# Kernel optimization log

Measured on AMD Instinct MI355X. Metric: run time of the kernel, lower is better.

The kernel has to match this reference:

```python
import jax, jax.numpy as jnp
import numpy as np

NUM_HEADS = 64
HEAD_DIM = 10  # forced by nn.Linear(10, 1)


def setup_inputs() -> dict:
    key = jax.random.key(0)
    kq, kk, kv, kw = jax.random.split(key, 4)
    B, T, M = 16, 4096, NUM_HEADS * HEAD_DIM
    return {
        "query": jax.random.normal(kq, (B, T, M), dtype=jnp.float32),
        "key": jax.random.normal(kk, (B, T, M), dtype=jnp.float32),
        "value": jax.random.normal(kv, (B, T, M), dtype=jnp.float32),
        "W": jax.random.normal(kw, (1, HEAD_DIM), dtype=jnp.float32) * 0.3,
        "b": jnp.zeros((1,), dtype=jnp.float32),
    }


def _to_heads(x):
    # torch: stack(split(x, head_dim, dim=2), dim=0) -> [H, B, T, D]
    B, T, M = x.shape
    return x.reshape(B, T, NUM_HEADS, HEAD_DIM).transpose(2, 0, 1, 3)


def reference(query, key, value, W, b):
    D = HEAD_DIM
    q = _to_heads(query)   # [H,B,T,D]
    k = _to_heads(key)     # [H,B,T,D]
    v = _to_heads(value)   # [H,B,T,D]
    # key.transpose(-1,-2).sum(3).unsqueeze(2): sum over T -> [H,B,1,D]
    k_sum = k.sum(axis=2, keepdims=True)
    attn = jax.nn.softmax(jnp.tanh(q * k_sum / np.float32(np.sqrt(D))), axis=-1)
    t = attn * v                          # [H,B,T,D]
    v_q = t.sum(axis=2)                   # [H,B,D]
    v_v = t.sum(axis=3).transpose(1, 0, 2)  # [B,H,T]
    # input_proj: Linear(10,1) on v_q*v_q (v_query == v_key == t summed over T)
    s = jnp.tanh((v_q * v_q) @ W.T + b)   # [H,B,1]
    s = jax.nn.softmax(s, axis=-1)        # softmax over size-1 dim (== ones)
    s = s.transpose(1, 0, 2)              # [B,H,1]
    return v_v * s                        # [B,H,T]
```

## Files before the change

### kernel.cpp

```cpp
#include <hip/hip_runtime.h>
#include <stdint.h>

#define BB 16
#define TT 4096
#define HH 64
#define MM 640

#define PADF4 41
#define ROWSF (PADF4 * 4)

__global__ void __launch_bounds__(256)
ksum_kernel(const float* __restrict__ key, float* __restrict__ ksum) {
    int g = blockIdx.x * blockDim.x + threadIdx.x;
    int b = g / 160;
    int c = g % 160;
    int t0 = blockIdx.y * 32;

    const float4* p = reinterpret_cast<const float4*>(key)
                    + (size_t)b * TT * 160 + (size_t)t0 * 160 + c;

    float4 a0 = make_float4(0.f,0.f,0.f,0.f);
    float4 a1 = make_float4(0.f,0.f,0.f,0.f);
    float4 a2 = make_float4(0.f,0.f,0.f,0.f);
    float4 a3 = make_float4(0.f,0.f,0.f,0.f);
    #pragma unroll
    for (int i = 0; i < 32; i += 4) {
        float4 x0 = p[(size_t)(i + 0) * 160];
        float4 x1 = p[(size_t)(i + 1) * 160];
        float4 x2 = p[(size_t)(i + 2) * 160];
        float4 x3 = p[(size_t)(i + 3) * 160];
        a0.x += x0.x; a0.y += x0.y; a0.z += x0.z; a0.w += x0.w;
        a1.x += x1.x; a1.y += x1.y; a1.z += x1.z; a1.w += x1.w;
        a2.x += x2.x; a2.y += x2.y; a2.z += x2.z; a2.w += x2.w;
        a3.x += x3.x; a3.y += x3.y; a3.z += x3.z; a3.w += x3.w;
    }
    float sx = (a0.x + a1.x) + (a2.x + a3.x);
    float sy = (a0.y + a1.y) + (a2.y + a3.y);
    float sz = (a0.z + a1.z) + (a2.z + a3.z);
    float sw = (a0.w + a1.w) + (a2.w + a3.w);

    float* dst = ksum + b * MM + c * 4;
    atomicAdd(dst + 0, sx);
    atomicAdd(dst + 1, sy);
    atomicAdd(dst + 2, sz);
    atomicAdd(dst + 3, sw);
}

__device__ __forceinline__ float tanh_rcp(float x) {
    float ax = fabsf(x);
    float e2 = __expf(-2.0f * ax);
    float th = (1.0f - e2) * __builtin_amdgcn_rcpf(1.0f + e2);
    return copysignf(th, x);
}

__global__ void __launch_bounds__(64)
attn_kernel(const float* __restrict__ q,
            const float* __restrict__ v,
            const float* __restrict__ ksum,
            float* __restrict__ out) {
    __shared__ float qs[8 * ROWSF];
    __shared__ float vs[8 * ROWSF];
    __shared__ float ks_lds[160];

    const int lane = threadIdx.x;
    const int bid  = blockIdx.x;
    const int part = bid & 63;
    const int hg   = (bid >> 6) & 3;
    const int b    = bid >> 8;

    if (lane < 40) {
        reinterpret_cast<float4*>(ks_lds)[lane] =
            reinterpret_cast<const float4*>(ksum + b * MM + hg * 160)[lane];
    }

    const int row = lane & 7;
    const int hq  = lane >> 3;

    int srow[5], scol[5];
    #pragma unroll
    for (int j = 0; j < 5; ++j) {
        int s = lane + 64 * j;
        srow[j] = s / 40;
        scol[j] = s % 40;
    }

    const float R = 0.316227766016838f;
    float ksr[2][10];
    #pragma unroll
    for (int o = 0; o < 2; ++o)
        #pragma unroll
        for (int d = 0; d < 10; ++d)
            ksr[o][d] = ks_lds[(hq + 8 * o) * 10 + d] * R;

    const float4* qg0 = reinterpret_cast<const float4*>(q)
                      + (size_t)b * TT * 160 + hg * 40;
    const float4* vg0 = reinterpret_cast<const float4*>(v)
                      + (size_t)b * TT * 160 + hg * 40;
    float* ob0 = out + ((size_t)(b * HH + hg * 16 + hq)) * TT;

    float4* qs4 = reinterpret_cast<float4*>(qs);
    float4* vs4 = reinterpret_cast<float4*>(vs);

    #pragma unroll 1
    for (int i = 0; i < 8; ++i) {
        const int t0 = part * 64 + i * 8;

        const float4* qg = qg0 + (size_t)t0 * 160;
        const float4* vg = vg0 + (size_t)t0 * 160;
        float4 rq[5], rv[5];
        #pragma unroll
        for (int j = 0; j < 5; ++j) {
            rq[j] = qg[srow[j] * 160 + scol[j]];
            rv[j] = vg[srow[j] * 160 + scol[j]];
        }
        #pragma unroll
        for (int j = 0; j < 5; ++j) {
            qs4[srow[j] * PADF4 + scol[j]] = rq[j];
            vs4[srow[j] * PADF4 + scol[j]] = rv[j];
        }

        #pragma unroll
        for (int o = 0; o < 2; ++o) {
            const int fb = row * ROWSF + (hq + 8 * o) * 10;
            const float2* qp2 = reinterpret_cast<const float2*>(qs + fb);
            const float2* vp2 = reinterpret_cast<const float2*>(vs + fb);
            float sum = 0.f, dot = 0.f;
            #pragma unroll
            for (int p = 0; p < 5; ++p) {
                float2 qq = qp2[p];
                float2 vv = vp2[p];
                float e0 = __expf(tanh_rcp(qq.x * ksr[o][2*p]));
                float e1 = __expf(tanh_rcp(qq.y * ksr[o][2*p+1]));
                sum += e0 + e1;
                dot += e0 * vv.x + e1 * vv.y;
            }
            ob0[(size_t)(8 * o) * TT + t0 + row]
                = dot * __builtin_amdgcn_rcpf(sum);
        }
    }
}

extern "C" void kernel_launch(void* const* d_in, const int* in_sizes, int n_in,
                              void* d_out, int out_size, void* d_ws, size_t ws_size,
                              hipStream_t stream) {
    const float* q = (const float*)d_in[0];
    const float* k = (const float*)d_in[1];
    const float* v = (const float*)d_in[2];
    float* out  = (float*)d_out;
    float* ksum = (float*)d_ws;

    hipMemsetAsync(d_ws, 0, (size_t)BB * MM * sizeof(float), stream);
    ksum_kernel<<<dim3(10, 128), dim3(256), 0, stream>>>(k, ksum);
    attn_kernel<<<dim3(4096), dim3(64), 0, stream>>>(q, v, ksum, out);
}
```

Measured before the change: 129.6 us.

## Use 4-wave blocks and register-prefetch next tile during compute in attn kernel

The attention kernel now runs 256-thread blocks, where each wave owns a private LDS slice and 32 time steps, on half as many blocks. It prefetches the next 8-row tile of q and v into registers before computing the current one, and writes them to LDS after the compute. Scheduling barriers keep the loads issued ahead of the math. The goal is to hide global load latency behind the exp/tanh work and to cut per-block overhead. The cost is more registers and fewer blocks, which could lower occupancy.

```diff
diff --git a/kernel.cpp b/kernel.cpp
--- a/kernel.cpp
+++ b/kernel.cpp
@@ -7,7 +7,8 @@
 #define MM 640
 
 #define PADF4 41
-#define ROWSF (PADF4 * 4)
+#define WROWS 8
+#define NITER 4
 
 __global__ void __launch_bounds__(256)
 ksum_kernel(const float* __restrict__ key, float* __restrict__ ksum) {
@@ -53,28 +54,39 @@
     return copysignf(th, x);
 }
 
-__global__ void __launch_bounds__(64)
+__global__ void __launch_bounds__(256)
 attn_kernel(const float* __restrict__ q,
             const float* __restrict__ v,
             const float* __restrict__ ksum,
             float* __restrict__ out) {
-    __shared__ float qs[8 * ROWSF];
-    __shared__ float vs[8 * ROWSF];
-    __shared__ float ks_lds[160];
+    __shared__ float4 qs4[4 * WROWS * PADF4];
+    __shared__ float4 vs4[4 * WROWS * PADF4];
+    __shared__ float4 ks4[4 * 40];
 
-    const int lane = threadIdx.x;
+    const int tid  = threadIdx.x;
+    const int w    = tid >> 6;
+    const int lane = tid & 63;
     const int bid  = blockIdx.x;
-    const int part = bid & 63;
-    const int hg   = (bid >> 6) & 3;
-    const int b    = bid >> 8;
+    const int chunk = bid & 31;
+    const int hg    = (bid >> 5) & 3;
+    const int b     = bid >> 7;
 
     if (lane < 40) {
-        reinterpret_cast<float4*>(ks_lds)[lane] =
+        ks4[w * 40 + lane] =
             reinterpret_cast<const float4*>(ksum + b * MM + hg * 160)[lane];
     }
 
-    const int row = lane & 7;
-    const int hq  = lane >> 3;
+    const int row   = lane & 7;
+    const int head0 = lane >> 3;
+
+    const float* ksw = reinterpret_cast<const float*>(&ks4[w * 40]);
+    const float R = 0.316227766016838f;
+    float ksr0[10], ksr1[10];
+    #pragma unroll
+    for (int d = 0; d < 10; ++d) {
+        ksr0[d] = ksw[head0 * 10 + d] * R;
+        ksr1[d] = ksw[(head0 + 8) * 10 + d] * R;
+    }
 
     int srow[5], scol[5];
     #pragma unroll
@@ -84,58 +96,72 @@
         scol[j] = s % 40;
     }
 
-    const float R = 0.316227766016838f;
-    float ksr[2][10];
-    #pragma unroll
-    for (int o = 0; o < 2; ++o)
-        #pragma unroll
-        for (int d = 0; d < 10; ++d)
-            ksr[o][d] = ks_lds[(hq + 8 * o) * 10 + d] * R;
+    const float4* qg = reinterpret_cast<const float4*>(q)
+                     + (size_t)b * TT * 160 + hg * 40;
+    const float4* vg = reinterpret_cast<const float4*>(v)
+                     + (size_t)b * TT * 160 + hg * 40;
 
-    const float4* qg0 = reinterpret_cast<const float4*>(q)
-                      + (size_t)b * TT * 160 + hg * 40;
-    const float4* vg0 = reinterpret_cast<const float4*>(v)
-                      + (size_t)b * TT * 160 + hg * 40;
-    float* ob0 = out + ((size_t)(b * HH + hg * 16 + hq)) * TT;
+    float4* qw = &qs4[w * (WROWS * PADF4)];
+    float4* vw = &vs4[w * (WROWS * PADF4)];
+    const float* qwf = reinterpret_cast<const float*>(qw);
+    const float* vwf = reinterpret_cast<const float*>(vw);
 
-    float4* qs4 = reinterpret_cast<float4*>(qs);
-    float4* vs4 = reinterpret_cast<float4*>(vs);
+    const int tw0 = chunk * 128 + w * 32;
+    float* ob = out + ((size_t)(b * HH + hg * 16)) * TT;
 
-    #pragma unroll 1
-    for (int i = 0; i < 8; ++i) {
-        const int t0 = part * 64 + i * 8;
-
-        const float4* qg = qg0 + (size_t)t0 * 160;
-        const float4* vg = vg0 + (size_t)t0 * 160;
-        float4 rq[5], rv[5];
+    float4 rq[5], rv[5];
+    {
+        const float4* qt = qg + (size_t)tw0 * 160;
+        const float4* vt = vg + (size_t)tw0 * 160;
         #pragma unroll
         for (int j = 0; j < 5; ++j) {
-            rq[j] = qg[srow[j] * 160 + scol[j]];
-            rv[j] = vg[srow[j] * 160 + scol[j]];
+            rq[j] = qt[srow[j] * 160 + scol[j]];
+            rv[j] = vt[srow[j] * 160 + scol[j]];
         }
         #pragma unroll
         for (int j = 0; j < 5; ++j) {
-            qs4[srow[j] * PADF4 + scol[j]] = rq[j];
-            vs4[srow[j] * PADF4 + scol[j]] = rv[j];
+            qw[srow[j] * PADF4 + scol[j]] = rq[j];
+            vw[srow[j] * PADF4 + scol[j]] = rv[j];
         }
+    }
+
+    #pragma unroll 1
+    for (int it = 0; it < NITER; ++it) {
+        const int t0 = tw0 + it * WROWS;
+
+        if (it + 1 < NITER) {
+            const float4* qt = qg + (size_t)(t0 + WROWS) * 160;
+            const float4* vt = vg + (size_t)(t0 + WROWS) * 160;
+            #pragma unroll
+            for (int j = 0; j < 5; ++j) {
+                rq[j] = qt[srow[j] * 160 + scol[j]];
+                rv[j] = vt[srow[j] * 160 + scol[j]];
+            }
+        }
+        __builtin_amdgcn_sched_barrier(0);
 
         #pragma unroll
         for (int o = 0; o < 2; ++o) {
-            const int fb = row * ROWSF + (hq + 8 * o) * 10;
-            const float2* qp2 = reinterpret_cast<const float2*>(qs + fb);
-            const float2* vp2 = reinterpret_cast<const float2*>(vs + fb);
+            const int head  = head0 + 8 * o;
+            const int fb    = row * (PADF4 * 4) + head * 10;
+            const float* kk = o ? ksr1 : ksr0;
             float sum = 0.f, dot = 0.f;
             #pragma unroll
-            for (int p = 0; p < 5; ++p) {
-                float2 qq = qp2[p];
-                float2 vv = vp2[p];
-                float e0 = __expf(tanh_rcp(qq.x * ksr[o][2*p]));
-                float e1 = __expf(tanh_rcp(qq.y * ksr[o][2*p+1]));
-                sum += e0 + e1;
-                dot += e0 * vv.x + e1 * vv.y;
+            for (int d = 0; d < 10; ++d) {
+                float e = __expf(tanh_rcp(qwf[fb + d] * kk[d]));
+                sum += e;
+                dot += e * vwf[fb + d];
             }
-            ob0[(size_t)(8 * o) * TT + t0 + row]
-                = dot * __builtin_amdgcn_rcpf(sum);
+            ob[(size_t)head * TT + t0 + row] = dot * __builtin_amdgcn_rcpf(sum);
+        }
+        __builtin_amdgcn_sched_barrier(0);
+
+        if (it + 1 < NITER) {
+            #pragma unroll
+            for (int j = 0; j < 5; ++j) {
+                qw[srow[j] * PADF4 + scol[j]] = rq[j];
+                vw[srow[j] * PADF4 + scol[j]] = rv[j];
+            }
         }
     }
 }
@@ -151,5 +177,5 @@
 
     hipMemsetAsync(d_ws, 0, (size_t)BB * MM * sizeof(float), stream);
     ksum_kernel<<<dim3(10, 128), dim3(256), 0, stream>>>(k, ksum);
-    attn_kernel<<<dim3(4096), dim3(64), 0, stream>>>(q, v, ksum, out);
+    attn_kernel<<<dim3(2048), dim3(256), 0, stream>>>(q, v, ksum, out);
 }
```

Result: slower. 188.9 us (+45.8%).
